# Kernel tuning notes

Hardware: AMD Instinct MI355X
Metric: run time of the kernel (lower is better)

The kernel has to match this reference:

```python
import jax, jax.numpy as jnp
import numpy as np

B, S, D = 2, 4096, 1024
H, DK = 16, 64          # heads, QK feature dim per head
DV = D // H             # output features per head = 64
QKV_OUT = (2 * DK + DV) * H  # 3072


def setup_inputs() -> dict:
    key = jax.random.key(0)
    k1, k2, k3, k4, k5 = jax.random.split(key, 5)
    x = jax.random.normal(k1, (B, S, D), dtype=jnp.float32)
    Wqkv = jax.random.normal(k2, (D, QKV_OUT), dtype=jnp.float32) * (1.0 / np.sqrt(D))
    bqkv = jnp.zeros((QKV_OUT,), dtype=jnp.float32)
    Wproj = jax.random.normal(k3, (D, D), dtype=jnp.float32) * (1.0 / np.sqrt(D))
    bproj = jnp.zeros((D,), dtype=jnp.float32)
    return {"x": x, "Wqkv": Wqkv, "bqkv": bqkv, "Wproj": Wproj, "bproj": bproj}


def reference(x, Wqkv, bqkv, Wproj, bproj):
    # QKV projection: [B,S,(2*DK+DV)*H]
    qkv = x @ Wqkv + bqkv
    q_len = DK * H
    Q = qkv[:, :, :q_len].reshape(B, S, H, DK).transpose(0, 2, 1, 3)        # [B,H,S,DK]
    K = qkv[:, :, q_len:2 * q_len].reshape(B, S, H, DK).transpose(0, 2, 1, 3)
    V = qkv[:, :, 2 * q_len:].reshape(B, S, H, DV).transpose(0, 2, 1, 3)    # [B,H,S,DV]

    scores = jnp.einsum("bhqd,bhkd->bhqk", Q, K) * (1.0 / np.sqrt(DK))
    # Faithful to source: causal mask is tril(ones) with zeros -> -inf,
    # i.e. +1.0 is ADDED on allowed positions (harmless constant shift per row).
    tril = jnp.tril(jnp.ones((S, S), dtype=jnp.float32))
    mask = jnp.where(tril == 0, -jnp.inf, tril)
    scores = scores + mask
    attn = jax.nn.softmax(scores, axis=-1)  # dropout disabled (p=0 / eval)

    out = jnp.einsum("bhqk,bhkd->bhqd", attn, V)            # [B,H,S,DV]
    out = out.transpose(0, 2, 1, 3).reshape(B, S, H * DV)   # [B,S,D]
    return out @ Wproj + bproj
```

## Files before the change

### kernel.cpp

```cpp
#include <hip/hip_runtime.h>
#include <stdint.h>


typedef __bf16 bf16x8 __attribute__((ext_vector_type(8)));
typedef float f32x4 __attribute__((ext_vector_type(4)));
typedef unsigned short u16x8 __attribute__((ext_vector_type(8)));
typedef unsigned short u16x4 __attribute__((ext_vector_type(4)));

__device__ __forceinline__ unsigned short f2bf(float f) {
  unsigned u = __builtin_bit_cast(unsigned, f);
  u += 0x7FFFu + ((u >> 16) & 1u);
  return (unsigned short)(u >> 16);
}

__device__ __forceinline__ float fast_exp2(float x) {
#if __has_builtin(__builtin_amdgcn_exp2f)
  return __builtin_amdgcn_exp2f(x);
#else
  return exp2f(x);
#endif
}

__device__ __forceinline__ void gload16(const void* g, void* l) {
  __builtin_amdgcn_global_load_lds(
      (__attribute__((address_space(1))) unsigned int*)(uintptr_t)g,
      (__attribute__((address_space(3))) unsigned int*)(unsigned int)(uintptr_t)l,
      16, 0, 0);
}

__global__ void k_cvt_bf16(const float* __restrict__ in,
                           unsigned short* __restrict__ out, int n8) {
  int i = blockIdx.x * blockDim.x + threadIdx.x;
  if (i >= n8) return;
  const float4* p = reinterpret_cast<const float4*>(in) + (size_t)i * 2;
  float4 a = p[0], b = p[1];
  u16x8 o;
  o[0] = f2bf(a.x); o[1] = f2bf(a.y); o[2] = f2bf(a.z); o[3] = f2bf(a.w);
  o[4] = f2bf(b.x); o[5] = f2bf(b.y); o[6] = f2bf(b.z); o[7] = f2bf(b.w);
  *(reinterpret_cast<u16x8*>(out) + i) = o;
}

__global__ void k_transcvt(const float* __restrict__ in,
                           unsigned short* __restrict__ out, int K, int N) {
  __shared__ float tile[32][33];
  int tk0 = blockIdx.y << 5, tn0 = blockIdx.x << 5;
  int t = threadIdx.x;
  int r = t >> 3, c4 = (t & 7) << 2;
  float4 v = *reinterpret_cast<const float4*>(&in[(size_t)(tk0 + r) * N + tn0 + c4]);
  tile[r][c4 + 0] = v.x; tile[r][c4 + 1] = v.y;
  tile[r][c4 + 2] = v.z; tile[r][c4 + 3] = v.w;
  __syncthreads();
  u16x4 o;
  o[0] = f2bf(tile[c4 + 0][r]); o[1] = f2bf(tile[c4 + 1][r]);
  o[2] = f2bf(tile[c4 + 2][r]); o[3] = f2bf(tile[c4 + 3][r]);
  *reinterpret_cast<u16x4*>(&out[(size_t)(tn0 + r) * K + tk0 + c4]) = o;
}

__device__ __forceinline__ void gemm_core(
    const unsigned short* __restrict__ A, const unsigned short* __restrict__ Bt,
    unsigned short* Al, unsigned short* Bl, int m0, int n0, f32x4 acc[4][4]) {
  const int t = threadIdx.x;
  const int lane = t & 63;
  const int w = t >> 6;
  const int wr = w >> 1, wc = w & 1;
  const int l15 = lane & 15, l4 = lane >> 4;

  const int c0 = t, c1 = t + 256;
  const int r0 = c0 >> 2, s0 = ((c0 & 3) << 3) ^ (((r0 >> 1) & 3) << 3);
  const int r1 = c1 >> 2, s1 = ((c1 & 3) << 3) ^ (((r1 >> 1) & 3) << 3);
  const size_t ga0 = (size_t)(m0 + r0) * 1024 + s0;
  const size_t ga1 = (size_t)(m0 + r1) * 1024 + s1;
  const size_t gb0 = (size_t)(n0 + r0) * 1024 + s0;
  const size_t gb1 = (size_t)(n0 + r1) * 1024 + s1;

  int aidx[4], bidx[4];
#pragma unroll
  for (int m = 0; m < 4; ++m) {
    int row = wr * 64 + m * 16 + l15;
    aidx[m] = row * 32 + ((l4 * 8) ^ (((row >> 1) & 3) << 3));
    row = wc * 64 + m * 16 + l15;
    bidx[m] = row * 32 + ((l4 * 8) ^ (((row >> 1) & 3) << 3));
  }

  for (int kk = 0; kk < 1024; kk += 32) {
    __syncthreads();
    gload16(A + ga0 + kk, Al + c0 * 8);
    gload16(A + ga1 + kk, Al + c1 * 8);
    gload16(Bt + gb0 + kk, Bl + c0 * 8);
    gload16(Bt + gb1 + kk, Bl + c1 * 8);
    __syncthreads();
    bf16x8 af[4], bfr[4];
#pragma unroll
    for (int m = 0; m < 4; ++m)
      af[m] = *reinterpret_cast<const bf16x8*>(Al + aidx[m]);
#pragma unroll
    for (int n = 0; n < 4; ++n)
      bfr[n] = *reinterpret_cast<const bf16x8*>(Bl + bidx[n]);
#pragma unroll
    for (int m = 0; m < 4; ++m)
#pragma unroll
      for (int n = 0; n < 4; ++n)
        acc[m][n] = __builtin_amdgcn_mfma_f32_16x16x32_bf16(af[m], bfr[n],
                                                            acc[m][n], 0, 0, 0);
  }
}

__global__ __launch_bounds__(256) void k_gemm_qkv(
    const unsigned short* __restrict__ A, const unsigned short* __restrict__ Bt,
    const float* __restrict__ bias, unsigned short* __restrict__ Qb,
    unsigned short* __restrict__ Kb, unsigned short* __restrict__ VTb) {
  __shared__ unsigned short Al[128 * 32];
  __shared__ unsigned short Bl[128 * 32];
  const int lane = threadIdx.x & 63, w = threadIdx.x >> 6;
  const int wr = w >> 1, wc = w & 1;
  const int l15 = lane & 15, l4 = lane >> 4;
  const int m0 = blockIdx.y << 7, n0 = blockIdx.x << 7;
  const float C1 = 0.18033688011112043f;

  f32x4 acc[4][4] = {};
  gemm_core(A, Bt, Al, Bl, m0, n0, acc);

#pragma unroll
  for (int m = 0; m < 4; ++m) {
#pragma unroll
    for (int n = 0; n < 4; ++n) {
#pragma unroll
      for (int j = 0; j < 4; ++j) {
        int row = m0 + wr * 64 + m * 16 + l4 * 4 + j;
        int col = n0 + wc * 64 + n * 16 + l15;
        float v = acc[m][n][j] + bias[col];
        int b = row >> 12, s = row & 4095;
        if (col < 1024) {
          int hh = col >> 6, d = col & 63;
          Qb[((size_t)(b * 16 + hh) * 4096 + s) * 64 + d] = f2bf(v * C1);
        } else if (col < 2048) {
          int cc = col - 1024; int hh = cc >> 6, d = cc & 63;
          Kb[((size_t)(b * 16 + hh) * 4096 + s) * 64 + d] = f2bf(v);
        } else {
          int cc = col - 2048; int hh = cc >> 6, d = cc & 63;
          VTb[((size_t)(b * 16 + hh) * 64 + d) * 4096 + s] = f2bf(v);
        }
      }
    }
  }
}

__global__ __launch_bounds__(256) void k_gemm_proj(
    const unsigned short* __restrict__ A, const unsigned short* __restrict__ Bt,
    const float* __restrict__ bias, float* __restrict__ out) {
  __shared__ unsigned short Al[128 * 32];
  __shared__ unsigned short Bl[128 * 32];
  const int lane = threadIdx.x & 63, w = threadIdx.x >> 6;
  const int wr = w >> 1, wc = w & 1;
  const int l15 = lane & 15, l4 = lane >> 4;
  const int m0 = blockIdx.y << 7, n0 = blockIdx.x << 7;

  f32x4 acc[4][4] = {};
  gemm_core(A, Bt, Al, Bl, m0, n0, acc);

#pragma unroll
  for (int m = 0; m < 4; ++m) {
#pragma unroll
    for (int n = 0; n < 4; ++n) {
#pragma unroll
      for (int j = 0; j < 4; ++j) {
        int row = m0 + wr * 64 + m * 16 + l4 * 4 + j;
        int col = n0 + wc * 64 + n * 16 + l15;
        out[(size_t)row * 1024 + col] = acc[m][n][j] + bias[col];
      }
    }
  }
}

__global__ __launch_bounds__(256, 2) void k_attn(
    const unsigned short* __restrict__ Qb, const unsigned short* __restrict__ Kb,
    const unsigned short* __restrict__ VTb, unsigned short* __restrict__ Ob) {
  __shared__ unsigned short Kl[2][64 * 64];
  __shared__ unsigned short Vl[2][64 * 64];
  __shared__ unsigned short Pl[4][32 * 36];
  const int t = threadIdx.x;
  const int lane = t & 63, w = t >> 6;
  const int l15 = lane & 15, l4 = lane >> 4;
  const int idx = blockIdx.x;
  const int jp = idx >> 5;
  const int bh = idx & 31;
  const size_t qkbase = (size_t)bh * 4096 * 64;
  const size_t vbase = (size_t)bh * 64 * 4096;
  const int b = bh >> 4, hh = bh & 15;

  const int c0 = t, c1 = t + 256;
  const int kr0 = c0 >> 3, ks0 = ((c0 & 7) << 3) ^ ((kr0 & 7) << 3);
  const int kr1 = c1 >> 3, ks1 = ((c1 & 7) << 3) ^ ((kr1 & 7) << 3);

#define STAGE(bufi, jt)                                                             \
  do {                                                                              \
    gload16(Kb + qkbase + (size_t)((jt) * 64 + kr0) * 64 + ks0, &Kl[bufi][c0 * 8]); \
    gload16(Kb + qkbase + (size_t)((jt) * 64 + kr1) * 64 + ks1, &Kl[bufi][c1 * 8]); \
    gload16(VTb + vbase + (size_t)kr0 * 4096 + (jt) * 64 + ks0, &Vl[bufi][c0 * 8]); \
    gload16(VTb + vbase + (size_t)kr1 * 4096 + (jt) * 64 + ks1, &Vl[bufi][c1 * 8]); \
  } while (0)

#define PV_HALF(kkh)                                                                \
  do {                                                                              \
    bf16x8 pf0 = *reinterpret_cast<const bf16x8*>(&Pl[w][(l15)*36 + l4 * 8]);       \
    bf16x8 pf1 = *reinterpret_cast<const bf16x8*>(&Pl[w][(16 + l15) * 36 + l4 * 8]);\
    __builtin_amdgcn_s_setprio(1);                                                  \
    _Pragma("unroll") for (int nn = 0; nn < 4; ++nn) {                              \
      int vr = nn * 16 + l15;                                                       \
      int vc = ((kkh) * 32 + l4 * 8) ^ ((vr & 7) << 3);                             \
      bf16x8 vf = *reinterpret_cast<const bf16x8*>(&Vl[cur][vr * 64 + vc]);         \
      oacc[0][nn] = __builtin_amdgcn_mfma_f32_16x16x32_bf16(pf0, vf,                \
                                                            oacc[0][nn], 0, 0, 0);  \
      oacc[1][nn] = __builtin_amdgcn_mfma_f32_16x16x32_bf16(pf1, vf,                \
                                                            oacc[1][nn], 0, 0, 0);  \
    }                                                                               \
    __builtin_amdgcn_s_setprio(0);                                                  \
  } while (0)

#pragma unroll 1
  for (int pass = 0; pass < 2; ++pass) {
    const int qt = pass ? (31 - jp) : jp;
    const int wrow0 = qt * 128 + w * 32;
    const int nt = 2 * qt + 2;

    bf16x8 qf[2][2];
#pragma unroll
    for (int m = 0; m < 2; ++m)
#pragma unroll
      for (int kk = 0; kk < 2; ++kk)
        qf[m][kk] = *reinterpret_cast<const bf16x8*>(
            &Qb[qkbase + (size_t)(wrow0 + m * 16 + l15) * 64 + kk * 32 + l4 * 8]);

    f32x4 oacc[2][4] = {};
    float lsum[2] = {};

    STAGE(0, 0);
    asm volatile("s_waitcnt vmcnt(0)" ::: "memory");
    __builtin_amdgcn_s_barrier();

    for (int j = 0; j < nt; ++j) {
      const int cur = j & 1;
      if (j + 1 < nt) STAGE(cur ^ 1, j + 1);

      const int jk0 = j * 64;
      const bool active = (jk0 <= wrow0 + 31);
      const bool needmask = active && (jk0 + 63 > wrow0);

      if (active) {
#pragma unroll
        for (int n = 0; n < 4; ++n) {
          f32x4 sc[2] = {};
          __builtin_amdgcn_s_setprio(1);
#pragma unroll
          for (int kk = 0; kk < 2; ++kk) {
            int krow = n * 16 + l15;
            int kcol = (kk * 32 + l4 * 8) ^ ((krow & 7) << 3);
            bf16x8 kfr = *reinterpret_cast<const bf16x8*>(&Kl[cur][krow * 64 + kcol]);
#pragma unroll
            for (int m = 0; m < 2; ++m)
              sc[m] = __builtin_amdgcn_mfma_f32_16x16x32_bf16(kfr, qf[m][kk],
                                                              sc[m], 0, 0, 0);
          }
          __builtin_amdgcn_s_setprio(0);

          const int colbase = (n & 1) * 16 + l4 * 4;
          if (needmask) {
            const int kb = jk0 + n * 16 + l4 * 4;
#pragma unroll
            for (int m = 0; m < 2; ++m) {
              const int qg = wrow0 + m * 16 + l15;
              u16x4 pk;
#pragma unroll
              for (int r = 0; r < 4; ++r) {
                float p = fast_exp2(sc[m][r]);
                if (kb + r > qg) p = 0.f;
                lsum[m] += p;
                pk[r] = __builtin_bit_cast(unsigned short, (__bf16)p);
              }
              *reinterpret_cast<u16x4*>(&Pl[w][(m * 16 + l15) * 36 + colbase]) = pk;
            }
          } else {
#pragma unroll
            for (int m = 0; m < 2; ++m) {
              u16x4 pk;
#pragma unroll
              for (int r = 0; r < 4; ++r) {
                float p = fast_exp2(sc[m][r]);
                lsum[m] += p;
                pk[r] = __builtin_bit_cast(unsigned short, (__bf16)p);
              }
              *reinterpret_cast<u16x4*>(&Pl[w][(m * 16 + l15) * 36 + colbase]) = pk;
            }
          }
          if (n == 1) PV_HALF(0);
          if (n == 3) PV_HALF(1);
        }
      }

      asm volatile("s_waitcnt vmcnt(0)" ::: "memory");
      __builtin_amdgcn_s_barrier();
    }

#pragma unroll
    for (int m = 0; m < 2; ++m) {
      lsum[m] += __shfl_xor(lsum[m], 16);
      lsum[m] += __shfl_xor(lsum[m], 32);
    }
#pragma unroll
    for (int m = 0; m < 2; ++m)
#pragma unroll
      for (int jj = 0; jj < 4; ++jj) {
        float inv = 1.0f / __shfl(lsum[m], l4 * 4 + jj);
        int srow = wrow0 + m * 16 + l4 * 4 + jj;
#pragma unroll
        for (int nn = 0; nn < 4; ++nn) {
          int col = hh * 64 + nn * 16 + l15;
          Ob[((size_t)(b * 4096 + srow)) * 1024 + col] =
              __builtin_bit_cast(unsigned short, (__bf16)(oacc[m][nn][jj] * inv));
        }
      }
  }
#undef STAGE
#undef PV_HALF
}

extern "C" void kernel_launch(void* const* d_in, const int* in_sizes, int n_in,
                              void* d_out, int out_size, void* d_ws, size_t ws_size,
                              hipStream_t stream) {
  const float* x = (const float*)d_in[0];
  const float* Wqkv = (const float*)d_in[1];
  const float* bqkv = (const float*)d_in[2];
  const float* Wproj = (const float*)d_in[3];
  const float* bproj = (const float*)d_in[4];

  char* ws = (char*)d_ws;
  unsigned short* xb  = (unsigned short*)(ws);
  unsigned short* Wqb = (unsigned short*)(ws + 16777216);
  unsigned short* Wpb = (unsigned short*)(ws + 23068672);
  unsigned short* Qb  = (unsigned short*)(ws + 25165824);
  unsigned short* Kb  = (unsigned short*)(ws + 41943040);
  unsigned short* VTb = (unsigned short*)(ws + 58720256);
  unsigned short* Ob  = (unsigned short*)(ws + 75497472);

  k_cvt_bf16<<<dim3(8388608 / 8 / 256), dim3(256), 0, stream>>>(x, xb, 8388608 / 8);
  k_transcvt<<<dim3(3072 / 32, 1024 / 32), dim3(256), 0, stream>>>(Wqkv, Wqb, 1024, 3072);
  k_transcvt<<<dim3(1024 / 32, 1024 / 32), dim3(256), 0, stream>>>(Wproj, Wpb, 1024, 1024);
  k_gemm_qkv<<<dim3(3072 / 128, 8192 / 128), dim3(256), 0, stream>>>(xb, Wqb, bqkv, Qb, Kb, VTb);
  k_attn<<<dim3(512), dim3(256), 0, stream>>>(Qb, Kb, VTb, Ob);
  k_gemm_proj<<<dim3(1024 / 128, 8192 / 128), dim3(256), 0, stream>>>(Ob, Wpb, bproj, (float*)d_out);
}
```

Measured before the change: 234.7 us.

## Keep attention probabilities in registers via permlane swaps and launch one Q tile per block

The attention kernel no longer writes P to LDS and reads it back. Scores are converted with packed bf16 conversion and rearranged across lanes with permlane32/permlane16 swaps so they can feed the PV MFMA directly. The two-pass pairing of a short and a long causal Q tile is replaced by one Q tile per block, with the grid doubled, heavier tiles launched first and launch bounds raised to 4 blocks per CU. This removes LDS traffic and its latency, and raises occupancy, at the cost of relying on the hardware scheduler to balance uneven causal work and on the correctness of the lane permutation.

Result: faster. 222.2 us (-5.3%).

```diff
diff --git a/kernel.cpp b/kernel.cpp
--- a/kernel.cpp
+++ b/kernel.cpp
@@ -6,6 +6,7 @@
 typedef float f32x4 __attribute__((ext_vector_type(4)));
 typedef unsigned short u16x8 __attribute__((ext_vector_type(8)));
 typedef unsigned short u16x4 __attribute__((ext_vector_type(4)));
+typedef unsigned int u32x4 __attribute__((ext_vector_type(4)));
 
 __device__ __forceinline__ unsigned short f2bf(float f) {
   unsigned u = __builtin_bit_cast(unsigned, f);
@@ -172,21 +173,22 @@
   }
 }
 
-__global__ __launch_bounds__(256, 2) void k_attn(
+__global__ __launch_bounds__(256, 4) void k_attn(
     const unsigned short* __restrict__ Qb, const unsigned short* __restrict__ Kb,
     const unsigned short* __restrict__ VTb, unsigned short* __restrict__ Ob) {
   __shared__ unsigned short Kl[2][64 * 64];
   __shared__ unsigned short Vl[2][64 * 64];
-  __shared__ unsigned short Pl[4][32 * 36];
   const int t = threadIdx.x;
   const int lane = t & 63, w = t >> 6;
   const int l15 = lane & 15, l4 = lane >> 4;
   const int idx = blockIdx.x;
-  const int jp = idx >> 5;
+  const int qt = 31 - (idx >> 5);
   const int bh = idx & 31;
   const size_t qkbase = (size_t)bh * 4096 * 64;
   const size_t vbase = (size_t)bh * 64 * 4096;
   const int b = bh >> 4, hh = bh & 15;
+  const int wrow0 = qt * 128 + w * 32;
+  const int nt = 2 * qt + 2;
 
   const int c0 = t, c1 = t + 256;
   const int kr0 = c0 >> 3, ks0 = ((c0 & 7) << 3) ^ ((kr0 & 7) << 3);
@@ -200,128 +202,129 @@
     gload16(VTb + vbase + (size_t)kr1 * 4096 + (jt) * 64 + ks1, &Vl[bufi][c1 * 8]); \
   } while (0)
 
-#define PV_HALF(kkh)                                                                \
-  do {                                                                              \
-    bf16x8 pf0 = *reinterpret_cast<const bf16x8*>(&Pl[w][(l15)*36 + l4 * 8]);       \
-    bf16x8 pf1 = *reinterpret_cast<const bf16x8*>(&Pl[w][(16 + l15) * 36 + l4 * 8]);\
-    __builtin_amdgcn_s_setprio(1);                                                  \
-    _Pragma("unroll") for (int nn = 0; nn < 4; ++nn) {                              \
-      int vr = nn * 16 + l15;                                                       \
-      int vc = ((kkh) * 32 + l4 * 8) ^ ((vr & 7) << 3);                             \
-      bf16x8 vf = *reinterpret_cast<const bf16x8*>(&Vl[cur][vr * 64 + vc]);         \
-      oacc[0][nn] = __builtin_amdgcn_mfma_f32_16x16x32_bf16(pf0, vf,                \
-                                                            oacc[0][nn], 0, 0, 0);  \
-      oacc[1][nn] = __builtin_amdgcn_mfma_f32_16x16x32_bf16(pf1, vf,                \
-                                                            oacc[1][nn], 0, 0, 0);  \
-    }                                                                               \
-    __builtin_amdgcn_s_setprio(0);                                                  \
-  } while (0)
-
-#pragma unroll 1
-  for (int pass = 0; pass < 2; ++pass) {
-    const int qt = pass ? (31 - jp) : jp;
-    const int wrow0 = qt * 128 + w * 32;
-    const int nt = 2 * qt + 2;
-
-    bf16x8 qf[2][2];
-#pragma unroll
-    for (int m = 0; m < 2; ++m)
-#pragma unroll
-      for (int kk = 0; kk < 2; ++kk)
-        qf[m][kk] = *reinterpret_cast<const bf16x8*>(
-            &Qb[qkbase + (size_t)(wrow0 + m * 16 + l15) * 64 + kk * 32 + l4 * 8]);
-
-    f32x4 oacc[2][4] = {};
-    float lsum[2] = {};
-
-    STAGE(0, 0);
+  bf16x8 qf[2][2];
+#pragma unroll
+  for (int m = 0; m < 2; ++m)
+#pragma unroll
+    for (int kk = 0; kk < 2; ++kk)
+      qf[m][kk] = *reinterpret_cast<const bf16x8*>(
+          &Qb[qkbase + (size_t)(wrow0 + m * 16 + l15) * 64 + kk * 32 + l4 * 8]);
+
+  f32x4 oacc[2][4] = {};
+  float lsum[2] = {};
+
+  STAGE(0, 0);
+  asm volatile("s_waitcnt vmcnt(0)" ::: "memory");
+  __builtin_amdgcn_s_barrier();
+
+  for (int j = 0; j < nt; ++j) {
+    const int cur = j & 1;
+    if (j + 1 < nt) STAGE(cur ^ 1, j + 1);
+
+    const int jk0 = j * 64;
+    const bool active = (jk0 <= wrow0 + 31);
+    const bool needmask = active && (jk0 + 63 > wrow0);
+
+    if (active) {
+#pragma unroll
+      for (int h = 0; h < 2; ++h) {
+        f32x4 sch[2][2] = {};
+        __builtin_amdgcn_s_setprio(1);
+#pragma unroll
+        for (int nn = 0; nn < 2; ++nn) {
+          int krow = (h * 2 + nn) * 16 + l15;
+#pragma unroll
+          for (int kk = 0; kk < 2; ++kk) {
+            int kcol = (kk * 32 + l4 * 8) ^ ((krow & 7) << 3);
+            bf16x8 kfr = *reinterpret_cast<const bf16x8*>(&Kl[cur][krow * 64 + kcol]);
+#pragma unroll
+            for (int m = 0; m < 2; ++m)
+              sch[m][nn] = __builtin_amdgcn_mfma_f32_16x16x32_bf16(
+                  kfr, qf[m][kk], sch[m][nn], 0, 0, 0);
+          }
+        }
+        __builtin_amdgcn_s_setprio(0);
+
+        bf16x8 pa[2];
+#pragma unroll
+        for (int m = 0; m < 2; ++m) {
+#pragma unroll
+          for (int nn = 0; nn < 2; ++nn)
+#pragma unroll
+            for (int r = 0; r < 4; ++r)
+              sch[m][nn][r] = fast_exp2(sch[m][nn][r]);
+          if (needmask) {
+            const int qg = wrow0 + m * 16 + l15;
+#pragma unroll
+            for (int nn = 0; nn < 2; ++nn) {
+              const int kb = jk0 + (h * 2 + nn) * 16 + l4 * 4;
+#pragma unroll
+              for (int r = 0; r < 4; ++r)
+                if (kb + r > qg) sch[m][nn][r] = 0.f;
+            }
+          }
+#pragma unroll
+          for (int nn = 0; nn < 2; ++nn)
+#pragma unroll
+            for (int r = 0; r < 4; ++r)
+              lsum[m] += sch[m][nn][r];
+
+          unsigned A0, A1, B0, B1;
+          asm("v_cvt_pk_bf16_f32 %0, %1, %2"
+              : "=v"(A0) : "v"(sch[m][0][0]), "v"(sch[m][0][1]));
+          asm("v_cvt_pk_bf16_f32 %0, %1, %2"
+              : "=v"(A1) : "v"(sch[m][0][2]), "v"(sch[m][0][3]));
+          asm("v_cvt_pk_bf16_f32 %0, %1, %2"
+              : "=v"(B0) : "v"(sch[m][1][0]), "v"(sch[m][1][1]));
+          asm("v_cvt_pk_bf16_f32 %0, %1, %2"
+              : "=v"(B1) : "v"(sch[m][1][2]), "v"(sch[m][1][3]));
+          asm("v_permlane32_swap_b32 %0, %1" : "+v"(A0), "+v"(B0));
+          asm("v_permlane16_swap_b32 %0, %1" : "+v"(A0), "+v"(B0));
+          asm("v_permlane32_swap_b32 %0, %1" : "+v"(A1), "+v"(B1));
+          asm("v_permlane16_swap_b32 %0, %1" : "+v"(A1), "+v"(B1));
+          u32x4 pw;
+          pw[0] = A0; pw[1] = A1; pw[2] = B0; pw[3] = B1;
+          pa[m] = __builtin_bit_cast(bf16x8, pw);
+        }
+
+        __builtin_amdgcn_s_setprio(1);
+#pragma unroll
+        for (int nn2 = 0; nn2 < 4; ++nn2) {
+          int vr = nn2 * 16 + l15;
+          int vc = (h * 32 + l4 * 8) ^ ((vr & 7) << 3);
+          bf16x8 vf = *reinterpret_cast<const bf16x8*>(&Vl[cur][vr * 64 + vc]);
+          oacc[0][nn2] = __builtin_amdgcn_mfma_f32_16x16x32_bf16(
+              pa[0], vf, oacc[0][nn2], 0, 0, 0);
+          oacc[1][nn2] = __builtin_amdgcn_mfma_f32_16x16x32_bf16(
+              pa[1], vf, oacc[1][nn2], 0, 0, 0);
+        }
+        __builtin_amdgcn_s_setprio(0);
+      }
+    }
+
     asm volatile("s_waitcnt vmcnt(0)" ::: "memory");
     __builtin_amdgcn_s_barrier();
-
-    for (int j = 0; j < nt; ++j) {
-      const int cur = j & 1;
-      if (j + 1 < nt) STAGE(cur ^ 1, j + 1);
-
-      const int jk0 = j * 64;
-      const bool active = (jk0 <= wrow0 + 31);
-      const bool needmask = active && (jk0 + 63 > wrow0);
-
-      if (active) {
-#pragma unroll
-        for (int n = 0; n < 4; ++n) {
-          f32x4 sc[2] = {};
-          __builtin_amdgcn_s_setprio(1);
-#pragma unroll
-          for (int kk = 0; kk < 2; ++kk) {
-            int krow = n * 16 + l15;
-            int kcol = (kk * 32 + l4 * 8) ^ ((krow & 7) << 3);
-            bf16x8 kfr = *reinterpret_cast<const bf16x8*>(&Kl[cur][krow * 64 + kcol]);
-#pragma unroll
-            for (int m = 0; m < 2; ++m)
-              sc[m] = __builtin_amdgcn_mfma_f32_16x16x32_bf16(kfr, qf[m][kk],
-                                                              sc[m], 0, 0, 0);
-          }
-          __builtin_amdgcn_s_setprio(0);
-
-          const int colbase = (n & 1) * 16 + l4 * 4;
-          if (needmask) {
-            const int kb = jk0 + n * 16 + l4 * 4;
-#pragma unroll
-            for (int m = 0; m < 2; ++m) {
-              const int qg = wrow0 + m * 16 + l15;
-              u16x4 pk;
-#pragma unroll
-              for (int r = 0; r < 4; ++r) {
-                float p = fast_exp2(sc[m][r]);
-                if (kb + r > qg) p = 0.f;
-                lsum[m] += p;
-                pk[r] = __builtin_bit_cast(unsigned short, (__bf16)p);
-              }
-              *reinterpret_cast<u16x4*>(&Pl[w][(m * 16 + l15) * 36 + colbase]) = pk;
-            }
-          } else {
-#pragma unroll
-            for (int m = 0; m < 2; ++m) {
-              u16x4 pk;
-#pragma unroll
-              for (int r = 0; r < 4; ++r) {
-                float p = fast_exp2(sc[m][r]);
-                lsum[m] += p;
-                pk[r] = __builtin_bit_cast(unsigned short, (__bf16)p);
-              }
-              *reinterpret_cast<u16x4*>(&Pl[w][(m * 16 + l15) * 36 + colbase]) = pk;
-            }
-          }
-          if (n == 1) PV_HALF(0);
-          if (n == 3) PV_HALF(1);
-        }
+  }
+#undef STAGE
+
+#pragma unroll
+  for (int m = 0; m < 2; ++m) {
+    lsum[m] += __shfl_xor(lsum[m], 16);
+    lsum[m] += __shfl_xor(lsum[m], 32);
+  }
+#pragma unroll
+  for (int m = 0; m < 2; ++m)
+#pragma unroll
+    for (int jj = 0; jj < 4; ++jj) {
+      float inv = 1.0f / __shfl(lsum[m], l4 * 4 + jj);
+      int srow = wrow0 + m * 16 + l4 * 4 + jj;
+#pragma unroll
+      for (int nn = 0; nn < 4; ++nn) {
+        int col = hh * 64 + nn * 16 + l15;
+        Ob[((size_t)(b * 4096 + srow)) * 1024 + col] =
+            __builtin_bit_cast(unsigned short, (__bf16)(oacc[m][nn][jj] * inv));
       }
-
-      asm volatile("s_waitcnt vmcnt(0)" ::: "memory");
-      __builtin_amdgcn_s_barrier();
     }
-
-#pragma unroll
-    for (int m = 0; m < 2; ++m) {
-      lsum[m] += __shfl_xor(lsum[m], 16);
-      lsum[m] += __shfl_xor(lsum[m], 32);
-    }
-#pragma unroll
-    for (int m = 0; m < 2; ++m)
-#pragma unroll
-      for (int jj = 0; jj < 4; ++jj) {
-        float inv = 1.0f / __shfl(lsum[m], l4 * 4 + jj);
-        int srow = wrow0 + m * 16 + l4 * 4 + jj;
-#pragma unroll
-        for (int nn = 0; nn < 4; ++nn) {
-          int col = hh * 64 + nn * 16 + l15;
-          Ob[((size_t)(b * 4096 + srow)) * 1024 + col] =
-              __builtin_bit_cast(unsigned short, (__bf16)(oacc[m][nn][jj] * inv));
-        }
-      }
-  }
-#undef STAGE
-#undef PV_HALF
 }
 
 extern "C" void kernel_launch(void* const* d_in, const int* in_sizes, int n_in,
@@ -346,6 +349,6 @@
   k_transcvt<<<dim3(3072 / 32, 1024 / 32), dim3(256), 0, stream>>>(Wqkv, Wqb, 1024, 3072);
   k_transcvt<<<dim3(1024 / 32, 1024 / 32), dim3(256), 0, stream>>>(Wproj, Wpb, 1024, 1024);
   k_gemm_qkv<<<dim3(3072 / 128, 8192 / 128), dim3(256), 0, stream>>>(xb, Wqb, bqkv, Qb, Kb, VTb);
-  k_attn<<<dim3(512), dim3(256), 0, stream>>>(Qb, Kb, VTb, Ob);
+  k_attn<<<dim3(1024), dim3(256), 0, stream>>>(Qb, Kb, VTb, Ob);
   k_gemm_proj<<<dim3(1024 / 128, 8192 / 128), dim3(256), 0, stream>>>(Ob, Wpb, bproj, (float*)d_out);
 }
```
